# Kernel optimization log

Hardware: AMD Instinct MI355X
Metric: run time of the kernel (lower is better)

## Reference

```python
import jax, jax.numpy as jnp
import numpy as np

EPS = 1e-12  # F.normalize eps


def _lstm_dir(x, Wih_d, Whh_d, b_d, reverse):
    # x: [M, dim]; Wih_d/Whh_d: [4*dim, dim]; b_d: [4*dim]
    dim = Whh_d.shape[1]
    def step(carry, xt):
        h, c = carry
        z = xt @ Wih_d.T + h @ Whh_d.T + b_d  # [4*dim]
        i, f, g, o = jnp.split(z, 4)
        i = jax.nn.sigmoid(i); f = jax.nn.sigmoid(f)
        g = jnp.tanh(g); o = jax.nn.sigmoid(o)
        c = f * c + i * g
        h = o * jnp.tanh(c)
        return (h, c), h
    init = (jnp.zeros((dim,), x.dtype), jnp.zeros((dim,), x.dtype))
    _, hs = jax.lax.scan(step, init, x, reverse=reverse)
    return hs  # [M, dim]


def _forward(fingerprints, adjacency, words, emb_fp, emb_word,
             Wg, bg, Wih, Whh, bih, bhh, Wc, bc, Wp, bp, Wo, bo, Wi, bi):
    # ---- GAT over compound graph ----
    xs = emb_fp[fingerprints]  # [N, dim]
    L_gat = Wg.shape[0]
    for i in range(L_gat):
        hs = jax.nn.relu(xs @ Wg[i].T + bg[i])          # [N, dim]
        w = hs @ hs.T                                    # [N, N]
        attn = w * adjacency
        denom = jnp.maximum(jnp.sum(jnp.abs(attn), axis=1, keepdims=True), EPS)
        xs = xs + (attn / denom) @ hs
    x = xs  # compound atom vectors [N, dim]

    # ---- bidirectional LSTM over protein words ----
    wv = emb_word[words]  # [M, dim]
    h_f = _lstm_dir(wv, Wih[0], Whh[0], bih[0] + bhh[0], reverse=False)
    h_b = _lstm_dir(wv, Wih[1], Whh[1], bih[1] + bhh[1], reverse=True)
    xs_rnn = jax.nn.relu(jnp.concatenate([h_f, h_b], axis=1))  # [M, 2*dim]

    # ---- cross attention pooling ----
    h = jax.nn.relu(x @ Wc.T + bc)         # [N, dim]
    hp = jax.nn.relu(xs_rnn @ Wp.T + bp)   # [M, dim]
    weights = h @ hp.T                     # [N, M]
    w_comp = jnp.mean(weights, axis=1)     # [N]  (mean over M)
    w_prot = jnp.mean(weights, axis=0)     # [M]
    y = w_comp[:, None] * h                # [N, dim]
    ys = w_prot[:, None] * hp              # [M, dim]
    compound_vector = jnp.mean(y, axis=0)[None, :]   # [1, dim]
    protein_vector = jnp.mean(ys, axis=0)[None, :]   # [1, dim]

    # ---- output MLP ----
    cat = jnp.concatenate([compound_vector, protein_vector], axis=1)  # [1, 2*dim]
    L_out = Wo.shape[0]
    for j in range(L_out):
        cat = jax.nn.relu(cat @ Wo[j].T + bo[j])
    interaction = cat @ Wi.T + bi  # [1, 2]
    return interaction, weights


def setup_inputs() -> dict:
    key = jax.random.key(0)
    ks = jax.random.split(key, 16)
    N, M, DIM = 4096, 4096, 128
    N_FP, N_WORD = 100000, 10000
    L_GAT, L_OUT = 3, 2
    s = 0.05
    return {
        "fingerprints": jax.random.randint(ks[0], (N,), 0, N_FP),
        "adjacency": jax.random.uniform(ks[1], (N, N), jnp.float32),
        "words": jax.random.randint(ks[2], (M,), 0, N_WORD),
        "emb_fp": jax.random.normal(ks[3], (N_FP, DIM), jnp.float32) * s,
        "emb_word": jax.random.normal(ks[4], (N_WORD, DIM), jnp.float32) * s,
        "Wg": jax.random.normal(ks[5], (L_GAT, DIM, DIM), jnp.float32) * s,
        "bg": jnp.zeros((L_GAT, DIM), jnp.float32),
        "Wih": jax.random.normal(ks[6], (2, 4 * DIM, DIM), jnp.float32) * s,
        "Whh": jax.random.normal(ks[7], (2, 4 * DIM, DIM), jnp.float32) * s,
        "bih": jnp.zeros((2, 4 * DIM), jnp.float32),
        "bhh": jnp.zeros((2, 4 * DIM), jnp.float32),
        "Wc": jax.random.normal(ks[8], (DIM, DIM), jnp.float32) * s,
        "bc": jnp.zeros((DIM,), jnp.float32),
        "Wp": jax.random.normal(ks[9], (DIM, 2 * DIM), jnp.float32) * s,
        "bp": jnp.zeros((DIM,), jnp.float32),
        "Wo": jax.random.normal(ks[10], (L_OUT, 2 * DIM, 2 * DIM), jnp.float32) * s,
        "bo": jnp.zeros((L_OUT, 2 * DIM), jnp.float32),
        "Wi": jax.random.normal(ks[11], (2, 2 * DIM), jnp.float32) * s,
        "bi": jnp.zeros((2,), jnp.float32),
    }


def reference(fingerprints, adjacency, words, emb_fp, emb_word,
              Wg, bg, Wih, Whh, bih, bhh, Wc, bc, Wp, bp, Wo, bo, Wi, bi):
    return _forward(fingerprints, adjacency, words, emb_fp, emb_word,
                    Wg, bg, Wih, Whh, bih, bhh, Wc, bc, Wp, bp, Wo, bo, Wi, bi)
```

## Files before the change

kernel.cpp:

```cpp
#include <hip/hip_runtime.h>
#include <hip/hip_bf16.h>
#include <math.h>

#define DIM 128

typedef float v2f __attribute__((ext_vector_type(2)));
typedef _Float16 v2h __attribute__((ext_vector_type(2)));
typedef short s8v __attribute__((ext_vector_type(8)));
typedef float f4v __attribute__((ext_vector_type(4)));

template<int CTRL>
__device__ inline float dpp_movf(float v) {
  int x = __builtin_amdgcn_update_dpp(0, __float_as_int(v), CTRL, 0xF, 0xF, true);
  return __int_as_float(x);
}
template<int CTRL>
__device__ inline float dpp_xadd(float v) { return v + dpp_movf<CTRL>(v); }

__device__ inline float dot8u(uint4 a, uint4 b, float acc) {
#if __has_builtin(__builtin_amdgcn_fdot2)
  acc = __builtin_amdgcn_fdot2(__builtin_bit_cast(v2h, a.x), __builtin_bit_cast(v2h, b.x), acc, false);
  acc = __builtin_amdgcn_fdot2(__builtin_bit_cast(v2h, a.y), __builtin_bit_cast(v2h, b.y), acc, false);
  acc = __builtin_amdgcn_fdot2(__builtin_bit_cast(v2h, a.z), __builtin_bit_cast(v2h, b.z), acc, false);
  acc = __builtin_amdgcn_fdot2(__builtin_bit_cast(v2h, a.w), __builtin_bit_cast(v2h, b.w), acc, false);
#else
  const v2h* pa = (const v2h*)&a; const v2h* pb = (const v2h*)&b;
#pragma unroll
  for (int i = 0; i < 4; ++i) {
    acc += (float)pa[i][0] * (float)pb[i][0];
    acc += (float)pa[i][1] * (float)pb[i][1];
  }
#endif
  return acc;
}

__device__ inline unsigned pk2h(float a, float b) {
  return __builtin_bit_cast(unsigned, __builtin_amdgcn_cvt_pkrtz(a, b));
}
__device__ inline float sigm_fast(float z) {
  return __builtin_amdgcn_rcpf(1.f + __expf(-z));
}
__device__ inline float tanh_fast(float z) {
  float e = __expf(-2.f * z);
  return (1.f - e) * __builtin_amdgcn_rcpf(1.f + e);
}
__device__ inline ushort f2bf(float x) {
  unsigned u = __builtin_bit_cast(unsigned, x);
  return (ushort)((u + 0x7FFFu + ((u >> 16) & 1u)) >> 16);
}

__global__ void gather_rows(const float* __restrict__ table, const int* __restrict__ idx,
                            float* __restrict__ dst, int n) {
  int i = blockIdx.x * blockDim.x + threadIdx.x;
  int total = n * 32;
  if (i >= total) return;
  int r = i >> 5, c = i & 31;
  const float4* src = (const float4*)table + (size_t)idx[r] * 32 + c;
  ((float4*)dst)[i] = *src;
}

template<bool RELU, bool HASBIAS, bool HASADJ, bool PERMB>
__global__ __launch_bounds__(256) void gemm_nt(
    const float* __restrict__ A, const float* __restrict__ B,
    float* __restrict__ C, int ldc, int K,
    const float* __restrict__ bias,
    const float* __restrict__ adj, int ldadj)
{
  __shared__ float As[64][17];
  __shared__ float Bs[64][17];
  int tid = threadIdx.x;
  int tx = tid & 15, ty = tid >> 4;
  int rowBase = blockIdx.y * 64, colBase = blockIdx.x * 64;
  int lr = tid >> 2, lk = (tid & 3) * 4;
  int brow = colBase + lr;
  if (PERMB) brow = 128 * (brow & 3) + (brow >> 2);
  float acc[4][4] = {};
  for (int k0 = 0; k0 < K; k0 += 16) {
    float4 av = *(const float4*)&A[(size_t)(rowBase + lr) * K + k0 + lk];
    float4 bv = *(const float4*)&B[(size_t)brow * K + k0 + lk];
    As[lr][lk+0]=av.x; As[lr][lk+1]=av.y; As[lr][lk+2]=av.z; As[lr][lk+3]=av.w;
    Bs[lr][lk+0]=bv.x; Bs[lr][lk+1]=bv.y; Bs[lr][lk+2]=bv.z; Bs[lr][lk+3]=bv.w;
    __syncthreads();
#pragma unroll
    for (int kk = 0; kk < 16; ++kk) {
      float a0=As[ty*4+0][kk], a1=As[ty*4+1][kk], a2=As[ty*4+2][kk], a3=As[ty*4+3][kk];
      float b0=Bs[tx*4+0][kk], b1=Bs[tx*4+1][kk], b2=Bs[tx*4+2][kk], b3=Bs[tx*4+3][kk];
      acc[0][0]+=a0*b0; acc[0][1]+=a0*b1; acc[0][2]+=a0*b2; acc[0][3]+=a0*b3;
      acc[1][0]+=a1*b0; acc[1][1]+=a1*b1; acc[1][2]+=a1*b2; acc[1][3]+=a1*b3;
      acc[2][0]+=a2*b0; acc[2][1]+=a2*b1; acc[2][2]+=a2*b2; acc[2][3]+=a2*b3;
      acc[3][0]+=a3*b0; acc[3][1]+=a3*b1; acc[3][2]+=a3*b2; acc[3][3]+=a3*b3;
    }
    __syncthreads();
  }
  int row = rowBase + ty*4, col = colBase + tx*4;
#pragma unroll
  for (int i = 0; i < 4; ++i) {
    float aj[4] = {1.f,1.f,1.f,1.f};
    if (HASADJ) {
      float4 adjv = *(const float4*)&adj[(size_t)(row+i)*ldadj + col];
      aj[0]=adjv.x; aj[1]=adjv.y; aj[2]=adjv.z; aj[3]=adjv.w;
    }
    float v[4];
#pragma unroll
    for (int j = 0; j < 4; ++j) {
      float x = acc[i][j];
      if (HASBIAS) {
        int bidx = col + j;
        if (PERMB) bidx = 128 * (bidx & 3) + (bidx >> 2);
        x += bias[bidx];
      }
      if (HASADJ) x *= aj[j];
      if (RELU) x = fmaxf(x, 0.f);
      v[j] = x;
    }
    float* cp = &C[(size_t)(row+i)*ldc + col];
    *(float2*)cp = make_float2(v[0], v[1]);
    *(float2*)(cp+2) = make_float2(v[2], v[3]);
  }
}

__global__ void conv_bf16_T(const float* __restrict__ src, ushort* __restrict__ d1,
                            ushort* __restrict__ dT, int n) {
  int i = blockIdx.x * blockDim.x + threadIdx.x;
  if (i >= n * DIM) return;
  int r = i >> 7, d = i & 127;
  ushort v = f2bf(src[i]);
  d1[i] = v;
  dT[(size_t)d * n + r] = v;
}

#define LDT 136
__global__ __launch_bounds__(256) void mfma_nt_adj(
    const ushort* __restrict__ A, const ushort* __restrict__ B,
    ushort* __restrict__ C, int ldc,
    const float* __restrict__ adj, int ldadj)
{
  __shared__ ushort As[128][LDT];
  __shared__ ushort Bs[128][LDT];
  int tid = threadIdx.x;
  int rowBase = blockIdx.y * 128, colBase = blockIdx.x * 128;
#pragma unroll
  for (int it = 0; it < 8; ++it) {
    int c = it * 256 + tid;
    int r = c >> 4, ch = (c & 15) * 8;
    *(uint4*)&As[r][ch] = *(const uint4*)&A[(size_t)(rowBase + r) * DIM + ch];
    *(uint4*)&Bs[r][ch] = *(const uint4*)&B[(size_t)(colBase + r) * DIM + ch];
  }
  __syncthreads();
  int lane = tid & 63;
  int wv = tid >> 6, wr = wv >> 1, wc = wv & 1;
  int lr = lane & 15, lk = (lane >> 4) * 8;
  f4v acc[4][4] = {};
#pragma unroll
  for (int kc = 0; kc < 4; ++kc) {
    s8v a[4], b[4];
#pragma unroll
    for (int i = 0; i < 4; ++i) {
      a[i] = *(const s8v*)&As[wr*64 + i*16 + lr][kc*32 + lk];
      b[i] = *(const s8v*)&Bs[wc*64 + i*16 + lr][kc*32 + lk];
    }
#pragma unroll
    for (int i = 0; i < 4; ++i)
#pragma unroll
      for (int j = 0; j < 4; ++j)
        acc[i][j] = __builtin_amdgcn_mfma_f32_16x16x32_bf16(a[i], b[j], acc[i][j], 0, 0, 0);
  }
  int rsub = (lane >> 4) * 4;
#pragma unroll
  for (int i = 0; i < 4; ++i)
#pragma unroll
    for (int j = 0; j < 4; ++j) {
      int col = colBase + wc*64 + j*16 + lr;
#pragma unroll
      for (int rg = 0; rg < 4; ++rg) {
        int row = rowBase + wr*64 + i*16 + rsub + rg;
        float v = acc[i][j][rg] * adj[(size_t)row * ldadj + col];
        C[(size_t)row * ldc + col] = f2bf(v);
      }
    }
}

#define LDT2 72
__global__ __launch_bounds__(256) void mfma_av(
    const ushort* __restrict__ attnb, const ushort* __restrict__ hsT,
    float* __restrict__ pt, int chunk, int N)
{
  __shared__ ushort As[128][LDT2];
  __shared__ ushort Bs[128][LDT2];
  int tid = threadIdx.x;
  int n0 = blockIdx.x * 128;
  int m0 = blockIdx.y * chunk;
  int lane = tid & 63;
  int wv = tid >> 6, wr = wv >> 1, wc = wv & 1;
  int lr = lane & 15, lk = (lane >> 4) * 8;
  f4v acc[4][4] = {};
  for (int mt = 0; mt < chunk; mt += 64) {
#pragma unroll
    for (int it = 0; it < 4; ++it) {
      int c = it * 256 + tid;
      int r = c >> 3, ch = (c & 7) * 8;
      *(uint4*)&As[r][ch] = *(const uint4*)&attnb[(size_t)(n0 + r) * N + m0 + mt + ch];
      *(uint4*)&Bs[r][ch] = *(const uint4*)&hsT[(size_t)r * N + m0 + mt + ch];
    }
    __syncthreads();
#pragma unroll
    for (int kc = 0; kc < 2; ++kc) {
      s8v a[4], b[4];
#pragma unroll
      for (int i = 0; i < 4; ++i) {
        a[i] = *(const s8v*)&As[wr*64 + i*16 + lr][kc*32 + lk];
        b[i] = *(const s8v*)&Bs[wc*64 + i*16 + lr][kc*32 + lk];
      }
#pragma unroll
      for (int i = 0; i < 4; ++i)
#pragma unroll
        for (int j = 0; j < 4; ++j)
          acc[i][j] = __builtin_amdgcn_mfma_f32_16x16x32_bf16(a[i], b[j], acc[i][j], 0, 0, 0);
    }
    __syncthreads();
  }
  size_t base = ((size_t)blockIdx.y * N + n0) * DIM;
  int rsub = (lane >> 4) * 4;
#pragma unroll
  for (int i = 0; i < 4; ++i)
#pragma unroll
    for (int j = 0; j < 4; ++j) {
      int d = wc*64 + j*16 + lr;
#pragma unroll
      for (int rg = 0; rg < 4; ++rg) {
        int nn = wr*64 + i*16 + rsub + rg;
        pt[base + (size_t)nn * DIM + d] = acc[i][j][rg];
      }
    }
}

__global__ void row_reduce_abs_bf16(const ushort* __restrict__ W, int ld, int M,
                                    float* __restrict__ out, float eps) {
  int n = blockIdx.x;
  const ushort* row = W + (size_t)n * ld;
  float s = 0;
  for (int m = threadIdx.x * 8; m < M; m += 256 * 8) {
    uint4 v = *(const uint4*)&row[m];
    unsigned a[4] = {v.x, v.y, v.z, v.w};
#pragma unroll
    for (int q = 0; q < 4; ++q) {
      s += __int_as_float((int)((a[q] & 0x7FFFu) << 16));
      s += __int_as_float((int)(a[q] & 0x7FFF0000u));
    }
  }
  __shared__ float red[256];
  red[threadIdx.x] = s; __syncthreads();
  for (int k = 128; k > 0; k >>= 1) {
    if (threadIdx.x < k) red[threadIdx.x] += red[threadIdx.x + k];
    __syncthreads();
  }
  if (threadIdx.x == 0) out[n] = fmaxf(red[0], eps);
}

__global__ void row_mean(const float* __restrict__ W, int ld, int M,
                         float* __restrict__ out, float inv) {
  int n = blockIdx.x;
  const float* row = W + (size_t)n * ld;
  float s = 0;
  for (int m = threadIdx.x; m < M; m += 256) s += row[m];
  __shared__ float red[256];
  red[threadIdx.x] = s; __syncthreads();
  for (int k = 128; k > 0; k >>= 1) {
    if (threadIdx.x < k) red[threadIdx.x] += red[threadIdx.x + k];
    __syncthreads();
  }
  if (threadIdx.x == 0) out[n] = red[0] * inv;
}

__global__ void colmean_part(const float* __restrict__ W, int ld, int rows_per,
                             float* __restrict__ part, int M) {
  int m = blockIdx.x * blockDim.x + threadIdx.x;
  int n0 = blockIdx.y * rows_per;
  float s = 0;
  for (int n = 0; n < rows_per; ++n) s += W[(size_t)(n0 + n) * ld + m];
  part[(size_t)blockIdx.y * M + m] = s;
}
__global__ void colmean_fin(const float* __restrict__ part, int M, int nparts,
                            float* __restrict__ out, float inv) {
  int m = blockIdx.x * blockDim.x + threadIdx.x;
  float s = 0;
  for (int k = 0; k < nparts; ++k) s += part[(size_t)k * M + m];
  out[m] = s * inv;
}

__global__ void axpy_reduce(const float* __restrict__ pt, const float* __restrict__ denom,
                            float* __restrict__ xs, int total) {
  int i = blockIdx.x * blockDim.x + threadIdx.x;
  if (i >= total) return;
  float s = 0;
#pragma unroll
  for (int k = 0; k < 8; ++k) s += pt[(size_t)k * total + i];
  xs[i] += s / denom[i >> 7];
}

__global__ void add_vec(const float* __restrict__ a, const float* __restrict__ b,
                        float* __restrict__ o, int n) {
  int i = blockIdx.x * blockDim.x + threadIdx.x;
  if (i < n) o[i] = a[i] + b[i];
}

#define REP8(X) X(0) X(1) X(2) X(3) X(4) X(5) X(6) X(7)

__global__ __launch_bounds__(512, 2) void lstm_kernel(
    const float* __restrict__ Whh,
    const float* __restrict__ Wxp,
    float* __restrict__ xs_rnn,
    int M)
{
  int dir = blockIdx.x;
  int tid = threadIdx.x;
  int w = tid >> 6, lane = tid & 63;
  int u  = w * 16 + (lane >> 2);
  int gp = (lane >> 1) & 1;
  int kh = lane & 1;
  int row0 = gp ? (256 + u) : u;
  const float* base = Whh + (size_t)dir * 512 * DIM;
  const float4* w0p = (const float4*)(base + (size_t)row0 * DIM + kh * 64);
  const float4* w1p = (const float4*)(base + (size_t)(row0 + 128) * DIM + kh * 64);

#define DECLW(r) uint4 wA##r, wB##r;
  REP8(DECLW)
#define LOADW(r) { \
    float4 x = w0p[2*(r)], y = w0p[2*(r)+1]; \
    wA##r = make_uint4(pk2h(x.x,x.y), pk2h(x.z,x.w), pk2h(y.x,y.y), pk2h(y.z,y.w)); \
    x = w1p[2*(r)]; y = w1p[2*(r)+1]; \
    wB##r = make_uint4(pk2h(x.x,x.y), pk2h(x.z,x.w), pk2h(y.x,y.y), pk2h(y.z,y.w)); }
  REP8(LOADW)

  __shared__ __align__(16) _Float16 hbuf[2][DIM];
  if (tid < DIM) hbuf[0][tid] = (_Float16)0.f;
  float c = 0.f;
  __syncthreads();

  const float* WxD = Wxp + (size_t)dir * M * 512;
  int wxcol = 4 * u + 2 * gp;
  int t0 = dir ? (M - 1) : 0;
  float2 wx = *(const float2*)&WxD[(size_t)t0 * 512 + wxcol];
  for (int s = 0; s < M; ++s) {
    int t = dir ? (M - 1 - s) : s;
    float2 wxn = make_float2(0.f, 0.f);
    if (s + 1 < M) {
      int tn = dir ? (M - 2 - s) : (s + 1);
      wxn = *(const float2*)&WxD[(size_t)tn * 512 + wxcol];
    }
    int cur = s & 1;
    const uint4* hb = (const uint4*)(hbuf[cur]) + kh * 8;
    float a0 = 0.f, a1 = 0.f;
#define DOTW(r) { uint4 hv = hb[r]; a0 = dot8u(wA##r, hv, a0); a1 = dot8u(wB##r, hv, a1); }
    REP8(DOTW)
    float z0 = dpp_xadd<0xB1>(a0) + wx.x;
    float z1 = dpp_xadd<0xB1>(a1) + wx.y;
    float av0 = gp ? tanh_fast(z0) : sigm_fast(z0);
    float av1 = sigm_fast(z1);
    float gv = dpp_movf<0x102>(av0);
    float ov = dpp_movf<0x102>(av1);
    if ((lane & 3) == 0) {
      c = av1 * c + av0 * gv;
      float hv = ov * tanh_fast(c);
      hbuf[cur ^ 1][u] = (_Float16)hv;
      xs_rnn[(size_t)t * (2 * DIM) + dir * DIM + u] = fmaxf(hv, 0.f);
    }
    wx = wxn;
    __syncthreads();
  }
#undef DOTW
#undef LOADW
#undef DECLW
}

__global__ void pool_vec(const float* __restrict__ mat, const float* __restrict__ wv,
                         int n, float* __restrict__ out, float inv) {
  int t = threadIdx.x; int g = t >> 7, d = t & 127;
  float acc = 0;
  for (int r = g; r < n; r += 8) acc += wv[r] * mat[(size_t)r * DIM + d];
  __shared__ float red[1024];
  red[t] = acc; __syncthreads();
  if (g == 0) {
    float s = acc;
#pragma unroll
    for (int k = 1; k < 8; ++k) s += red[k * 128 + d];
    out[d] = s * inv;
  }
}

__global__ void mlp_kernel(const float* __restrict__ cvec, const float* __restrict__ pvec,
                           const float* __restrict__ Wo, const float* __restrict__ bo,
                           const float* __restrict__ Wi, const float* __restrict__ bi,
                           float* __restrict__ out) {
  __shared__ float buf0[256], buf1[256];
  int t = threadIdx.x;
  buf0[t] = (t < 128) ? cvec[t] : pvec[t - 128];
  __syncthreads();
  {
    const float* W = Wo;
    float s = bo[t];
    for (int v = 0; v < 256; ++v) s += W[t * 256 + v] * buf0[v];
    buf1[t] = fmaxf(s, 0.f);
  }
  __syncthreads();
  {
    const float* W = Wo + 256 * 256;
    float s = bo[256 + t];
    for (int v = 0; v < 256; ++v) s += W[t * 256 + v] * buf1[v];
    buf0[t] = fmaxf(s, 0.f);
  }
  __syncthreads();
  if (t < 2) {
    float s = bi[t];
    for (int v = 0; v < 256; ++v) s += Wi[t * 256 + v] * buf0[v];
    out[t] = s;
  }
}

extern "C" void kernel_launch(void* const* d_in, const int* in_sizes, int n_in,
                              void* d_out, int out_size, void* d_ws, size_t ws_size,
                              hipStream_t stream) {
  const int*   fingerprints = (const int*)d_in[0];
  const float* adjacency    = (const float*)d_in[1];
  const int*   words        = (const int*)d_in[2];
  const float* emb_fp       = (const float*)d_in[3];
  const float* emb_word     = (const float*)d_in[4];
  const float* Wg  = (const float*)d_in[5];
  const float* bg  = (const float*)d_in[6];
  const float* Wih = (const float*)d_in[7];
  const float* Whh = (const float*)d_in[8];
  const float* bih = (const float*)d_in[9];
  const float* bhh = (const float*)d_in[10];
  const float* Wc  = (const float*)d_in[11];
  const float* bc  = (const float*)d_in[12];
  const float* Wp  = (const float*)d_in[13];
  const float* bp  = (const float*)d_in[14];
  const float* Wo  = (const float*)d_in[15];
  const float* bo  = (const float*)d_in[16];
  const float* Wi  = (const float*)d_in[17];
  const float* bi  = (const float*)d_in[18];

  const int N = in_sizes[0];
  const int M = in_sizes[2];
  const int LGAT = in_sizes[5] / (DIM * DIM);

  float* out  = (float*)d_out;
  float* attn = out + 2;
  ushort* attnb = (ushort*)attn;

  float* ws = (float*)d_ws;
  size_t off = 0;
  auto alloc = [&](size_t nf) { float* p = ws + off; off += (nf + 3) & ~(size_t)3; return p; };
  float* xs     = alloc((size_t)N * DIM);
  float* hs     = alloc((size_t)N * DIM);
  float* wvb    = alloc((size_t)M * DIM);
  float* denom  = alloc(N);
  float* pt     = alloc((size_t)8 * N * DIM);
  float* Wx     = pt;
  float* xs_rnn = alloc((size_t)M * 2 * DIM);
  float* hp     = alloc((size_t)M * DIM);
  float* hmat   = alloc((size_t)N * DIM);
  float* bsum   = alloc(1024);
  float* wcomp  = alloc(N);
  float* wprot  = alloc(M);
  float* cvec   = alloc(DIM);
  float* pvec   = alloc(DIM);
  float* cpart  = alloc((size_t)32 * M);
  ushort* hs_b  = (ushort*)alloc((size_t)N * DIM / 2);
  ushort* hsT_b = (ushort*)alloc((size_t)N * DIM / 2);
  (void)ws_size; (void)n_in; (void)out_size;

  gather_rows<<<(N * 32 + 255) / 256, 256, 0, stream>>>(emb_fp, fingerprints, xs, N);
  gather_rows<<<(M * 32 + 255) / 256, 256, 0, stream>>>(emb_word, words, wvb, M);

  for (int l = 0; l < LGAT; ++l) {
    gemm_nt<true, true, false, false><<<dim3(DIM / 64, N / 64), 256, 0, stream>>>(
        xs, Wg + (size_t)l * DIM * DIM, hs, DIM, DIM, bg + l * DIM, nullptr, 0);
    conv_bf16_T<<<(N * DIM) / 256, 256, 0, stream>>>(hs, hs_b, hsT_b, N);
    mfma_nt_adj<<<dim3(N / 128, N / 128), 256, 0, stream>>>(
        hs_b, hs_b, attnb, N, adjacency, N);
    row_reduce_abs_bf16<<<N, 256, 0, stream>>>(attnb, N, N, denom, 1e-12f);
    mfma_av<<<dim3(N / 128, 8), 256, 0, stream>>>(attnb, hsT_b, pt, N / 8, N);
    axpy_reduce<<<(N * DIM) / 256, 256, 0, stream>>>(pt, denom, xs, N * DIM);
  }

  add_vec<<<4, 256, 0, stream>>>(bih, bhh, bsum, 1024);
  for (int d = 0; d < 2; ++d) {
    gemm_nt<false, true, false, true><<<dim3(512 / 64, M / 64), 256, 0, stream>>>(
        wvb, Wih + (size_t)d * 512 * DIM, Wx + (size_t)d * M * 512, 512, DIM,
        bsum + d * 512, nullptr, 0);
  }
  lstm_kernel<<<2, 512, 0, stream>>>(Whh, Wx, xs_rnn, M);

  gemm_nt<true, true, false, false><<<dim3(DIM / 64, M / 64), 256, 0, stream>>>(
      xs_rnn, Wp, hp, DIM, 2 * DIM, bp, nullptr, 0);
  gemm_nt<true, true, false, false><<<dim3(DIM / 64, N / 64), 256, 0, stream>>>(
      xs, Wc, hmat, DIM, DIM, bc, nullptr, 0);
  gemm_nt<false, false, false, false><<<dim3(M / 64, N / 64), 256, 0, stream>>>(
      hmat, hp, attn, M, DIM, nullptr, nullptr, 0);
  row_mean<<<N, 256, 0, stream>>>(attn, M, M, wcomp, 1.f / (float)M);
  colmean_part<<<dim3(M / 256, 32), 256, 0, stream>>>(attn, M, N / 32, cpart, M);
  colmean_fin<<<M / 256, 256, 0, stream>>>(cpart, M, 32, wprot, 1.f / (float)N);
  pool_vec<<<1, 1024, 0, stream>>>(hmat, wcomp, N, cvec, 1.f / (float)N);
  pool_vec<<<1, 1024, 0, stream>>>(hp, wprot, M, pvec, 1.f / (float)M);

  mlp_kernel<<<1, 256, 0, stream>>>(cvec, pvec, Wo, bo, Wi, bi, out);
}
```

Before: 2.997 ms.

## Compute LSTM recurrent matvec with MFMA 16x16x32 f16 instead of fdot2

Replaces the per-lane fdot2 dot products in the sequential LSTM recurrence with MFMA 16x16x32 f16 instructions. The hidden vector is broadcast as the B operand and the Whh gate rows are held in registers as the A operands. Each lane picks out its unit's four gate values from the accumulator columns, so the DPP gate exchange goes away and every lane computes the cell update. The goal is to shorten the per-step latency of the serial recurrence, at the cost of redundant MFMA columns (the B vector is replicated) and a different Wx column layout.

```diff
diff --git a/kernel.cpp b/kernel.cpp
--- a/kernel.cpp
+++ b/kernel.cpp
@@ -6,6 +6,7 @@
 
 typedef float v2f __attribute__((ext_vector_type(2)));
 typedef _Float16 v2h __attribute__((ext_vector_type(2)));
+typedef _Float16 h8v __attribute__((ext_vector_type(8)));
 typedef short s8v __attribute__((ext_vector_type(8)));
 typedef float f4v __attribute__((ext_vector_type(4)));
 
@@ -17,23 +18,6 @@
 template<int CTRL>
 __device__ inline float dpp_xadd(float v) { return v + dpp_movf<CTRL>(v); }
 
-__device__ inline float dot8u(uint4 a, uint4 b, float acc) {
-#if __has_builtin(__builtin_amdgcn_fdot2)
-  acc = __builtin_amdgcn_fdot2(__builtin_bit_cast(v2h, a.x), __builtin_bit_cast(v2h, b.x), acc, false);
-  acc = __builtin_amdgcn_fdot2(__builtin_bit_cast(v2h, a.y), __builtin_bit_cast(v2h, b.y), acc, false);
-  acc = __builtin_amdgcn_fdot2(__builtin_bit_cast(v2h, a.z), __builtin_bit_cast(v2h, b.z), acc, false);
-  acc = __builtin_amdgcn_fdot2(__builtin_bit_cast(v2h, a.w), __builtin_bit_cast(v2h, b.w), acc, false);
-#else
-  const v2h* pa = (const v2h*)&a; const v2h* pb = (const v2h*)&b;
-#pragma unroll
-  for (int i = 0; i < 4; ++i) {
-    acc += (float)pa[i][0] * (float)pb[i][0];
-    acc += (float)pa[i][1] * (float)pb[i][1];
-  }
-#endif
-  return acc;
-}
-
 __device__ inline unsigned pk2h(float a, float b) {
   return __builtin_bit_cast(unsigned, __builtin_amdgcn_cvt_pkrtz(a, b));
 }
@@ -47,6 +31,11 @@
 __device__ inline ushort f2bf(float x) {
   unsigned u = __builtin_bit_cast(unsigned, x);
   return (ushort)((u + 0x7FFFu + ((u >> 16) & 1u)) >> 16);
+}
+__device__ inline float sel4(f4v v, int r) {
+  float t0 = (r & 1) ? v[1] : v[0];
+  float t1 = (r & 1) ? v[3] : v[2];
+  return (r & 2) ? t1 : t0;
 }
 
 __global__ void gather_rows(const float* __restrict__ table, const int* __restrict__ idx,
@@ -304,8 +293,6 @@
   if (i < n) o[i] = a[i] + b[i];
 }
 
-#define REP8(X) X(0) X(1) X(2) X(3) X(4) X(5) X(6) X(7)
-
 __global__ __launch_bounds__(512, 2) void lstm_kernel(
     const float* __restrict__ Whh,
     const float* __restrict__ Wxp,
@@ -315,62 +302,65 @@
   int dir = blockIdx.x;
   int tid = threadIdx.x;
   int w = tid >> 6, lane = tid & 63;
-  int u  = w * 16 + (lane >> 2);
-  int gp = (lane >> 1) & 1;
-  int kh = lane & 1;
-  int row0 = gp ? (256 + u) : u;
+  int lr = lane & 15, lq = lane >> 4;
+  h8v a[4][4];
   const float* base = Whh + (size_t)dir * 512 * DIM;
-  const float4* w0p = (const float4*)(base + (size_t)row0 * DIM + kh * 64);
-  const float4* w1p = (const float4*)(base + (size_t)(row0 + 128) * DIM + kh * 64);
-
-#define DECLW(r) uint4 wA##r, wB##r;
-  REP8(DECLW)
-#define LOADW(r) { \
-    float4 x = w0p[2*(r)], y = w0p[2*(r)+1]; \
-    wA##r = make_uint4(pk2h(x.x,x.y), pk2h(x.z,x.w), pk2h(y.x,y.y), pk2h(y.z,y.w)); \
-    x = w1p[2*(r)]; y = w1p[2*(r)+1]; \
-    wB##r = make_uint4(pk2h(x.x,x.y), pk2h(x.z,x.w), pk2h(y.x,y.y), pk2h(y.z,y.w)); }
-  REP8(LOADW)
-
+#pragma unroll
+  for (int g = 0; g < 4; ++g) {
+    const float* rp = base + (size_t)(g * 128 + w * 16 + lr) * DIM;
+#pragma unroll
+    for (int kt = 0; kt < 4; ++kt) {
+      const float4* p = (const float4*)(rp + kt * 32 + lq * 8);
+      float4 x = p[0], y = p[1];
+      h8v t;
+      t[0]=(_Float16)x.x; t[1]=(_Float16)x.y; t[2]=(_Float16)x.z; t[3]=(_Float16)x.w;
+      t[4]=(_Float16)y.x; t[5]=(_Float16)y.y; t[6]=(_Float16)y.z; t[7]=(_Float16)y.w;
+      a[g][kt] = t;
+    }
+  }
   __shared__ __align__(16) _Float16 hbuf[2][DIM];
   if (tid < DIM) hbuf[0][tid] = (_Float16)0.f;
+  int rsel = lr & 3;
+  int U = w * 16 + lq * 4 + rsel;
   float c = 0.f;
   __syncthreads();
 
   const float* WxD = Wxp + (size_t)dir * M * 512;
-  int wxcol = 4 * u + 2 * gp;
   int t0 = dir ? (M - 1) : 0;
-  float2 wx = *(const float2*)&WxD[(size_t)t0 * 512 + wxcol];
+  float4 wx = *(const float4*)&WxD[(size_t)t0 * 512 + 4 * U];
   for (int s = 0; s < M; ++s) {
     int t = dir ? (M - 1 - s) : s;
-    float2 wxn = make_float2(0.f, 0.f);
+    float4 wxn = make_float4(0.f, 0.f, 0.f, 0.f);
     if (s + 1 < M) {
       int tn = dir ? (M - 2 - s) : (s + 1);
-      wxn = *(const float2*)&WxD[(size_t)tn * 512 + wxcol];
+      wxn = *(const float4*)&WxD[(size_t)tn * 512 + 4 * U];
     }
     int cur = s & 1;
-    const uint4* hb = (const uint4*)(hbuf[cur]) + kh * 8;
-    float a0 = 0.f, a1 = 0.f;
-#define DOTW(r) { uint4 hv = hb[r]; a0 = dot8u(wA##r, hv, a0); a1 = dot8u(wB##r, hv, a1); }
-    REP8(DOTW)
-    float z0 = dpp_xadd<0xB1>(a0) + wx.x;
-    float z1 = dpp_xadd<0xB1>(a1) + wx.y;
-    float av0 = gp ? tanh_fast(z0) : sigm_fast(z0);
-    float av1 = sigm_fast(z1);
-    float gv = dpp_movf<0x102>(av0);
-    float ov = dpp_movf<0x102>(av1);
-    if ((lane & 3) == 0) {
-      c = av1 * c + av0 * gv;
-      float hv = ov * tanh_fast(c);
-      hbuf[cur ^ 1][u] = (_Float16)hv;
-      xs_rnn[(size_t)t * (2 * DIM) + dir * DIM + u] = fmaxf(hv, 0.f);
+    f4v acc0 = {0.f,0.f,0.f,0.f}, acc1 = {0.f,0.f,0.f,0.f};
+    f4v acc2 = {0.f,0.f,0.f,0.f}, acc3 = {0.f,0.f,0.f,0.f};
+#pragma unroll
+    for (int kt = 0; kt < 4; ++kt) {
+      h8v b = *(const h8v*)&hbuf[cur][kt * 32 + lq * 8];
+      acc0 = __builtin_amdgcn_mfma_f32_16x16x32_f16(a[0][kt], b, acc0, 0, 0, 0);
+      acc1 = __builtin_amdgcn_mfma_f32_16x16x32_f16(a[1][kt], b, acc1, 0, 0, 0);
+      acc2 = __builtin_amdgcn_mfma_f32_16x16x32_f16(a[2][kt], b, acc2, 0, 0, 0);
+      acc3 = __builtin_amdgcn_mfma_f32_16x16x32_f16(a[3][kt], b, acc3, 0, 0, 0);
+    }
+    float zi = sel4(acc0, rsel) + wx.x;
+    float zf = sel4(acc1, rsel) + wx.y;
+    float zg = sel4(acc2, rsel) + wx.z;
+    float zo = sel4(acc3, rsel) + wx.w;
+    float iv = sigm_fast(zi), fv = sigm_fast(zf);
+    float gv = tanh_fast(zg), ov = sigm_fast(zo);
+    c = fv * c + iv * gv;
+    float hv = ov * tanh_fast(c);
+    if (lr < 4) {
+      hbuf[cur ^ 1][U] = (_Float16)hv;
+      xs_rnn[(size_t)t * (2 * DIM) + dir * DIM + U] = fmaxf(hv, 0.f);
     }
     wx = wxn;
     __syncthreads();
   }
-#undef DOTW
-#undef LOADW
-#undef DECLW
 }
 
 __global__ void pool_vec(const float* __restrict__ mat, const float* __restrict__ wv,
```

After: 3.071 ms. 1.02x slower.
